# Performance work log

Hardware: AMD Instinct MI355X
Metric: run time of the kernel (lower is better)

## Reference

```python
import jax, jax.numpy as jnp
import numpy as np

NUM_NODES = 50000
NUM_EDGES = 600000
NUM_FEAT = 128
HIDDEN = 512
N_OUT = 128
K = 3
N_GRAPHS = 128


def setup_inputs() -> dict:
    key = jax.random.key(0)
    ks = jax.random.split(key, 12)
    feature = jax.random.normal(ks[0], (NUM_NODES, NUM_FEAT), dtype=jnp.float32)
    edge_index = jax.random.randint(ks[1], (2, NUM_EDGES), 0, NUM_NODES, dtype=jnp.int64)
    protein_batch = jnp.sort(jax.random.randint(ks[2], (NUM_NODES,), 0, N_GRAPHS, dtype=jnp.int64))
    s = 0.05
    # ChebConv weights stored [K, in, out] (x @ W), single shared bias per conv
    W1 = jax.random.normal(ks[3], (K, NUM_FEAT, NUM_FEAT), dtype=jnp.float32) * s
    b1 = jax.random.normal(ks[4], (NUM_FEAT,), dtype=jnp.float32) * s
    W2 = jax.random.normal(ks[5], (K, NUM_FEAT, 2 * NUM_FEAT), dtype=jnp.float32) * s
    b2 = jax.random.normal(ks[6], (2 * NUM_FEAT,), dtype=jnp.float32) * s
    fc1_w = jax.random.normal(ks[7], (3 * NUM_FEAT, HIDDEN), dtype=jnp.float32) * s
    fc1_b = jax.random.normal(ks[8], (HIDDEN,), dtype=jnp.float32) * s
    fc2_w = jax.random.normal(ks[9], (HIDDEN, N_OUT), dtype=jnp.float32) * s
    fc2_b = jax.random.normal(ks[10], (N_OUT,), dtype=jnp.float32) * s
    return {"feature": feature, "edge_index": edge_index, "protein_batch": protein_batch,
            "W1": W1, "b1": b1, "W2": W2, "b2": b2,
            "fc1_w": fc1_w, "fc1_b": fc1_b, "fc2_w": fc2_w, "fc2_b": fc2_b}


def _cheb_conv(x, src, dst, edge_w, W, b):
    # PyG ChebConv with sym normalization, lambda_max=2 => scaled Laplacian
    # L_hat has zero diagonal and off-diag weights -1/sqrt(d_i d_j) (edge_w).
    def prop(h):
        return jax.ops.segment_sum(edge_w[:, None] * h[src], dst, num_segments=NUM_NODES)

    Tx0 = x
    out = Tx0 @ W[0]
    Tx1 = prop(x)
    out = out + Tx1 @ W[1]
    for k in range(2, W.shape[0]):
        Tx2 = 2.0 * prop(Tx1) - Tx0
        out = out + Tx2 @ W[k]
        Tx0, Tx1 = Tx1, Tx2
    return out + b


def reference(feature, edge_index, protein_batch, W1, b1, W2, b2, fc1_w, fc1_b, fc2_w, fc2_b):
    src, dst = edge_index[0], edge_index[1]
    deg = jax.ops.segment_sum(jnp.ones_like(src, dtype=feature.dtype), src, num_segments=NUM_NODES)
    dinv = jnp.where(deg > 0, jax.lax.rsqrt(jnp.maximum(deg, 1.0)), 0.0)
    edge_w = -dinv[src] * dinv[dst]  # (2/lambda_max)*L_sym off-diagonal; diag cancels to 0

    gx = jax.nn.relu(_cheb_conv(feature, src, dst, edge_w, W1, b1))
    gx = jax.nn.relu(_cheb_conv(gx, src, dst, edge_w, W2, b2))
    gx = jnp.concatenate([gx, feature], axis=1)  # [N, 3*F]

    # global_mean_pool
    sums = jax.ops.segment_sum(gx, protein_batch, num_segments=N_GRAPHS)
    cnts = jax.ops.segment_sum(jnp.ones((gx.shape[0],), gx.dtype), protein_batch, num_segments=N_GRAPHS)
    pooled = sums / jnp.maximum(cnts, 1.0)[:, None]

    h = jax.nn.relu(pooled @ fc1_w + fc1_b)  # dropout is identity in eval
    return h @ fc2_w + fc2_b
```

## Files before the change

### kernel.cpp

```cpp
#include <hip/hip_runtime.h>
#include <hip/hip_bf16.h>

#define NNODES 50000
#define NEDGES 600000
#define NB 196
#define NBKT 196
#define SB 192
#define SCH (NEDGES / SB)

typedef short vs8 __attribute__((ext_vector_type(8)));
typedef float floatx4 __attribute__((ext_vector_type(4)));

__device__ __forceinline__ float us2f(unsigned short u) {
    unsigned int x = ((unsigned int)u) << 16;
    float f;
    __builtin_memcpy(&f, &x, 4);
    return f;
}
__device__ __forceinline__ unsigned short f2us(float f) {
    unsigned int x;
    __builtin_memcpy(&x, &f, 4);
    unsigned int r = x + 0x7fffu + ((x >> 16) & 1u);
    return (unsigned short)(r >> 16);
}
__device__ __forceinline__ float ldf(const void* p, int i, int ff) {
    if (ff) return us2f(((const unsigned short*)p)[i]);
    return ((const float*)p)[i];
}
__device__ __forceinline__ int2 ldnt_sw(const int2* p) {
    unsigned long long v =
        __builtin_nontemporal_load(reinterpret_cast<const unsigned long long*>(p));
    int2 r;
    r.x = (int)(unsigned int)(v & 0xffffffffULL);
    r.y = (int)(unsigned int)(v >> 32);
    return r;
}
__device__ __forceinline__ void accum8(float w, uint4 u, float& a0, float& a1,
                                       float& a2, float& a3, float& a4, float& a5,
                                       float& a6, float& a7) {
    a0 += w * us2f((unsigned short)(u.x & 0xffffu));
    a1 += w * us2f((unsigned short)(u.x >> 16));
    a2 += w * us2f((unsigned short)(u.y & 0xffffu));
    a3 += w * us2f((unsigned short)(u.y >> 16));
    a4 += w * us2f((unsigned short)(u.z & 0xffffu));
    a5 += w * us2f((unsigned short)(u.z >> 16));
    a6 += w * us2f((unsigned short)(u.w & 0xffffu));
    a7 += w * us2f((unsigned short)(u.w >> 16));
}

__global__ void k_detect(const int* ei, const unsigned int* fw, int* iflag, int* fflag) {
    int lane = threadIdx.x;
    int odd1 = ei[2 * lane + 1];
    int odd2 = ei[128 + 2 * lane + 1];
    unsigned long long nz = __ballot(odd1 != 0 || odd2 != 0);
    unsigned int e = (fw[lane] >> 7) & 0xffu;
    unsigned long long h = __ballot(e > 100u && e < 160u);
    if (lane == 0) {
        *iflag = (nz == 0ULL) ? 1 : 0;
        *fflag = (__popcll(h) > 40) ? 1 : 0;
    }
}

__global__ void k_init(const int* pb, const int* iflag, int* b32, float* psum) {
    int i = blockIdx.x * 256 + threadIdx.x;
    if (i < NNODES) {
        int f = *iflag;
        b32[i] = pb[((size_t)i) << f];
    }
    if (i < 128 * 384) psum[i] = 0.f;
}

__global__ __launch_bounds__(256) void k_deghist(const int* ei, const int* iflag,
                                                 unsigned int* degpart, int* cntpart) {
    __shared__ unsigned int h[25000];
    __shared__ int c[NBKT];
    int t = threadIdx.x, blk = blockIdx.x;
    for (int i = t; i < 25000; i += 256) h[i] = 0u;
    if (t < NBKT) c[t] = 0;
    __syncthreads();
    int f = *iflag;
    int e0 = blk * SCH;
    for (int j = t; j < SCH; j += 256) {
        int e = e0 + j;
        int s = ei[((size_t)e) << f];
        int d = ei[((size_t)(NEDGES + e)) << f];
        atomicAdd(&h[s >> 1], (s & 1) ? 65536u : 1u);
        atomicAdd(&c[d >> 8], 1);
    }
    __syncthreads();
    unsigned int* dp = degpart + (size_t)blk * 25000;
    for (int i = t; i < 25000; i += 256) dp[i] = h[i];
    if (t < NBKT) cntpart[blk * NBKT + t] = c[t];
}

__global__ void k_dred(const unsigned int* degpart, float* dinv) {
    int i = blockIdx.x * 256 + threadIdx.x;
    if (i >= 25000) return;
    unsigned int lo = 0, hi = 0;
    for (int b = 0; b < SB; ++b) {
        unsigned int p = degpart[(size_t)b * 25000 + i];
        lo += p & 0xffffu;
        hi += p >> 16;
    }
    dinv[2 * i] = lo ? rsqrtf((float)lo) : 0.f;
    dinv[2 * i + 1] = hi ? rsqrtf((float)hi) : 0.f;
}

__global__ void k_bscan(const int* cntpart, int* bbase, int* gbase,
                        const int* batch32, int* pcnt, int* rowptr) {
    __shared__ int tot[256];
    int t = threadIdx.x;
    int sum = 0;
    if (t < NBKT) {
        for (int b = 0; b < SB; ++b) sum += cntpart[b * NBKT + t];
    }
    tot[t] = sum;
    __syncthreads();
    for (int off = 1; off < 256; off <<= 1) {
        int x = (t >= off) ? tot[t - off] : 0;
        __syncthreads();
        tot[t] += x;
        __syncthreads();
    }
    int excl = tot[t] - sum;
    if (t < NBKT) {
        gbase[t] = excl;
        int run = excl;
        for (int b = 0; b < SB; ++b) {
            bbase[b * NBKT + t] = run;
            run += cntpart[b * NBKT + t];
        }
    }
    if (t == 0) {
        gbase[NBKT] = NEDGES;
        rowptr[NNODES] = NEDGES;
    }
    if (t < 128) {
        int g = t;
        int lo = 0, hi = NNODES;
        while (lo < hi) { int mid = (lo + hi) >> 1; if (batch32[mid] < g) lo = mid + 1; else hi = mid; }
        int start = lo;
        hi = NNODES;
        while (lo < hi) { int mid = (lo + hi) >> 1; if (batch32[mid] <= g) lo = mid + 1; else hi = mid; }
        pcnt[g] = lo - start;
    }
}

__global__ void k_scat(const int* ei, const int* iflag, const float* dinv,
                       const int* bbase, int2* bkt) {
    __shared__ int cur[NBKT];
    int t = threadIdx.x, blk = blockIdx.x;
    if (t < NBKT) cur[t] = bbase[blk * NBKT + t];
    __syncthreads();
    int f = *iflag;
    int e0 = blk * SCH;
    for (int j = t; j < SCH; j += 256) {
        int e = e0 + j;
        int s = ei[((size_t)e) << f];
        int d = ei[((size_t)(NEDGES + e)) << f];
        float w = -dinv[s] * dinv[d];
        int slot = atomicAdd(&cur[d >> 8], 1);
        int wb;
        __builtin_memcpy(&wb, &w, 4);
        int2 v;
        v.x = s | ((d & 255) << 16);
        v.y = wb;
        bkt[slot] = v;
    }
}

__global__ void k_csr(const int2* bkt, const int* gbase, int* rowptr, int2* csr_sw) {
    __shared__ int hist[256], scan[256], cur[256];
    int t = threadIdx.x, b = blockIdx.x;
    int beg = gbase[b], end = gbase[b + 1];
    int n = end - beg;
    hist[t] = 0;
    __syncthreads();
    for (int i = t; i < n; i += 256) {
        int bin = (bkt[beg + i].x >> 16) & 255;
        atomicAdd(&hist[bin], 1);
    }
    __syncthreads();
    int h = hist[t];
    scan[t] = h;
    __syncthreads();
    for (int off = 1; off < 256; off <<= 1) {
        int x = (t >= off) ? scan[t - off] : 0;
        __syncthreads();
        scan[t] += x;
        __syncthreads();
    }
    int excl = scan[t] - h;
    int node = b * 256 + t;
    if (node < NNODES) rowptr[node] = beg + excl;
    cur[t] = excl;
    __syncthreads();
    for (int i = t; i < n; i += 256) {
        int2 p = bkt[beg + i];
        int bin = (p.x >> 16) & 255;
        int slot = atomicAdd(&cur[bin], 1);
        int2 v;
        v.x = p.x & 0xffff;
        v.y = p.y;
        csr_sw[beg + slot] = v;
    }
}

__global__ void k_featb(const void* src, const int* fflag, unsigned short* dst) {
    int i = blockIdx.x * 256 + threadIdx.x;
    if (i >= NNODES * 128 / 8) return;
    if (*fflag) {
        reinterpret_cast<uint4*>(dst)[i] = reinterpret_cast<const uint4*>(src)[i];
    } else {
        const float4* fs = reinterpret_cast<const float4*>(src);
        float4 a = fs[2 * i], b = fs[2 * i + 1];
        uint4 o;
        o.x = (unsigned int)f2us(a.x) | ((unsigned int)f2us(a.y) << 16);
        o.y = (unsigned int)f2us(a.z) | ((unsigned int)f2us(a.w) << 16);
        o.z = (unsigned int)f2us(b.x) | ((unsigned int)f2us(b.y) << 16);
        o.w = (unsigned int)f2us(b.z) | ((unsigned int)f2us(b.w) << 16);
        reinterpret_cast<uint4*>(dst)[i] = o;
    }
}

__global__ void k_trans2(const void* W1, const void* W2, const int* fflag,
                         unsigned short* W1t, unsigned short* W2t) {
    int idx = blockIdx.x * 256 + threadIdx.x;
    int ff = *fflag;
    if (idx < 49152) {
        int n = idx / 384, k = idx - n * 384;
        float v;
        if (k < 128) v = ldf(W1, k * 128 + n, ff) - ldf(W1, (256 + k) * 128 + n, ff);
        else if (k < 256) v = ldf(W1, k * 128 + n, ff);
        else v = 2.f * ldf(W1, k * 128 + n, ff);
        W1t[idx] = f2us(v);
    } else if (idx < 49152 + 98304) {
        int j = idx - 49152;
        int n = j / 384, k = j - n * 384;
        float v;
        if (k < 128) v = ldf(W2, k * 256 + n, ff) - ldf(W2, (256 + k) * 256 + n, ff);
        else if (k < 256) v = ldf(W2, k * 256 + n, ff);
        else v = 2.f * ldf(W2, k * 256 + n, ff);
        W2t[j] = f2us(v);
    }
}

__global__ void k_prepw(const void* b1, const void* b2, const void* f1w, const void* f1b,
                        const void* f2w, const void* f2b, const int* fflag,
                        float* b1f, float* b2f, float* f1wf, float* f1bf,
                        float* f2wf, float* f2bf) {
    int i = blockIdx.x * 256 + threadIdx.x;
    int ff = *fflag;
    if (i < 196608) { f1wf[i] = ldf(f1w, i, ff); return; }
    i -= 196608;
    if (i < 65536) { f2wf[i] = ldf(f2w, i, ff); return; }
    i -= 65536;
    if (i < 512) { f1bf[i] = ldf(f1b, i, ff); return; }
    i -= 512;
    if (i < 256) { b2f[i] = ldf(b2, i, ff); return; }
    i -= 256;
    if (i < 128) { b1f[i] = ldf(b1, i, ff); return; }
    i -= 128;
    if (i < 128) f2bf[i] = ldf(f2b, i, ff);
}

__global__ __launch_bounds__(256, 4) void k_prop(const unsigned short* X,
                                                 const int* rowptr, const int2* csr_sw,
                                                 unsigned short* out) {
    int wvid = (blockIdx.x * blockDim.x + threadIdx.x) >> 6;
    int lane = threadIdx.x & 63;
    int q = lane >> 4;
    int ln = lane & 15;
    int node = wvid * 4 + q;
    if (node >= NNODES) return;
    int fo = ln * 8;
    int beg = rowptr[node], end = rowptr[node + 1];
    float a0 = 0.f, a1 = 0.f, a2 = 0.f, a3 = 0.f;
    float a4 = 0.f, a5 = 0.f, a6 = 0.f, a7 = 0.f;
    int j = beg;
    for (; j + 8 <= end; j += 8) {
        int2 e0 = ldnt_sw(csr_sw + j);
        int2 e1 = ldnt_sw(csr_sw + j + 1);
        int2 e2 = ldnt_sw(csr_sw + j + 2);
        int2 e3 = ldnt_sw(csr_sw + j + 3);
        int2 e4 = ldnt_sw(csr_sw + j + 4);
        int2 e5 = ldnt_sw(csr_sw + j + 5);
        int2 e6 = ldnt_sw(csr_sw + j + 6);
        int2 e7 = ldnt_sw(csr_sw + j + 7);
        uint4 u0 = *reinterpret_cast<const uint4*>(X + (size_t)e0.x * 128 + fo);
        uint4 u1 = *reinterpret_cast<const uint4*>(X + (size_t)e1.x * 128 + fo);
        uint4 u2 = *reinterpret_cast<const uint4*>(X + (size_t)e2.x * 128 + fo);
        uint4 u3 = *reinterpret_cast<const uint4*>(X + (size_t)e3.x * 128 + fo);
        uint4 u4 = *reinterpret_cast<const uint4*>(X + (size_t)e4.x * 128 + fo);
        uint4 u5 = *reinterpret_cast<const uint4*>(X + (size_t)e5.x * 128 + fo);
        uint4 u6 = *reinterpret_cast<const uint4*>(X + (size_t)e6.x * 128 + fo);
        uint4 u7 = *reinterpret_cast<const uint4*>(X + (size_t)e7.x * 128 + fo);
        float w0, w1, w2, w3, w4, w5, w6, w7;
        __builtin_memcpy(&w0, &e0.y, 4);
        __builtin_memcpy(&w1, &e1.y, 4);
        __builtin_memcpy(&w2, &e2.y, 4);
        __builtin_memcpy(&w3, &e3.y, 4);
        __builtin_memcpy(&w4, &e4.y, 4);
        __builtin_memcpy(&w5, &e5.y, 4);
        __builtin_memcpy(&w6, &e6.y, 4);
        __builtin_memcpy(&w7, &e7.y, 4);
        accum8(w0, u0, a0, a1, a2, a3, a4, a5, a6, a7);
        accum8(w1, u1, a0, a1, a2, a3, a4, a5, a6, a7);
        accum8(w2, u2, a0, a1, a2, a3, a4, a5, a6, a7);
        accum8(w3, u3, a0, a1, a2, a3, a4, a5, a6, a7);
        accum8(w4, u4, a0, a1, a2, a3, a4, a5, a6, a7);
        accum8(w5, u5, a0, a1, a2, a3, a4, a5, a6, a7);
        accum8(w6, u6, a0, a1, a2, a3, a4, a5, a6, a7);
        accum8(w7, u7, a0, a1, a2, a3, a4, a5, a6, a7);
    }
    for (; j + 4 <= end; j += 4) {
        int2 e0 = ldnt_sw(csr_sw + j);
        int2 e1 = ldnt_sw(csr_sw + j + 1);
        int2 e2 = ldnt_sw(csr_sw + j + 2);
        int2 e3 = ldnt_sw(csr_sw + j + 3);
        uint4 u0 = *reinterpret_cast<const uint4*>(X + (size_t)e0.x * 128 + fo);
        uint4 u1 = *reinterpret_cast<const uint4*>(X + (size_t)e1.x * 128 + fo);
        uint4 u2 = *reinterpret_cast<const uint4*>(X + (size_t)e2.x * 128 + fo);
        uint4 u3 = *reinterpret_cast<const uint4*>(X + (size_t)e3.x * 128 + fo);
        float w0, w1, w2, w3;
        __builtin_memcpy(&w0, &e0.y, 4);
        __builtin_memcpy(&w1, &e1.y, 4);
        __builtin_memcpy(&w2, &e2.y, 4);
        __builtin_memcpy(&w3, &e3.y, 4);
        accum8(w0, u0, a0, a1, a2, a3, a4, a5, a6, a7);
        accum8(w1, u1, a0, a1, a2, a3, a4, a5, a6, a7);
        accum8(w2, u2, a0, a1, a2, a3, a4, a5, a6, a7);
        accum8(w3, u3, a0, a1, a2, a3, a4, a5, a6, a7);
    }
    for (; j < end; ++j) {
        int2 e = ldnt_sw(csr_sw + j);
        float w;
        __builtin_memcpy(&w, &e.y, 4);
        uint4 u = *reinterpret_cast<const uint4*>(X + (size_t)e.x * 128 + fo);
        accum8(w, u, a0, a1, a2, a3, a4, a5, a6, a7);
    }
    uint4 ov;
    ov.x = (unsigned int)f2us(a0) | ((unsigned int)f2us(a1) << 16);
    ov.y = (unsigned int)f2us(a2) | ((unsigned int)f2us(a3) << 16);
    ov.z = (unsigned int)f2us(a4) | ((unsigned int)f2us(a5) << 16);
    ov.w = (unsigned int)f2us(a6) | ((unsigned int)f2us(a7) << 16);
    *reinterpret_cast<uint4*>(out + (size_t)node * 128 + fo) = ov;
}

template <int POOL>
__global__ __launch_bounds__(512, 4) void k_convg(
    const unsigned short* seg0, const unsigned short* seg1, const unsigned short* seg2,
    const unsigned short* Wt, const float* bias, unsigned short* out,
    const int* batch32, float* psum, int nout, int nslab) {
    __shared__ unsigned short shb[24576];
    __shared__ float sh_ps[512];
    int tid = threadIdx.x;
    int bid = blockIdx.x;
    int grp = 8 * nslab;
    int main_blocks = 24 * grp;
    int r, slab;
    if (bid < main_blocks) {
        int g = bid / grp;
        int rem = bid - g * grp;
        slab = rem >> 3;
        r = g * 8 + (rem & 7);
    } else {
        int t = bid - main_blocks;
        r = 192 + (t & 3);
        slab = t >> 2;
    }
    int col0 = slab * 64;
    if (POOL) sh_ps[tid] = 0.f;
#pragma unroll
    for (int it = 0; it < 6; ++it) {
        int idx = tid + it * 512;
        int kkt = idx >> 6, ln = idx & 63;
        int kk = kkt >> 2, t = kkt & 3;
        int col = col0 + t * 16 + (ln & 15);
        int ko = kk * 32 + (ln >> 4) * 8;
        uint4 v = *reinterpret_cast<const uint4*>(Wt + (size_t)col * 384 + ko);
        *reinterpret_cast<uint4*>(shb + idx * 8) = v;
    }
    __syncthreads();
    int wv = tid >> 6, lane = tid & 63;
    int m = lane & 15, kq = lane >> 4;
    int row0 = r * 256 + wv * 32;
    int rr0 = row0 + m;
    int rr1 = row0 + 16 + m;
    if (rr0 >= NNODES) rr0 = NNODES - 1;
    if (rr1 >= NNODES) rr1 = NNODES - 1;
    floatx4 acc[2][4];
#pragma unroll
    for (int rI = 0; rI < 2; ++rI)
#pragma unroll
        for (int t = 0; t < 4; ++t) {
            acc[rI][t][0] = 0.f; acc[rI][t][1] = 0.f; acc[rI][t][2] = 0.f; acc[rI][t][3] = 0.f;
        }
    vs8 a0[12], a1[12];
#pragma unroll
    for (int p = 0; p < 4; ++p) {
        int ko = p * 32 + kq * 8;
        a0[p] = *reinterpret_cast<const vs8*>(seg0 + (size_t)rr0 * 128 + ko);
        a1[p] = *reinterpret_cast<const vs8*>(seg0 + (size_t)rr1 * 128 + ko);
    }
    __builtin_amdgcn_sched_barrier(0);
#pragma unroll
    for (int kk = 0; kk < 12; ++kk) {
        int kp = kk + 4;
        if (kp < 12) {
            const unsigned short* S = (kp < 8) ? seg1 : seg2;
            int ko = (kp & 3) * 32 + kq * 8;
            a0[kp] = *reinterpret_cast<const vs8*>(S + (size_t)rr0 * 128 + ko);
            a1[kp] = *reinterpret_cast<const vs8*>(S + (size_t)rr1 * 128 + ko);
            __builtin_amdgcn_sched_barrier(0);
        }
#pragma unroll
        for (int t = 0; t < 4; ++t) {
            vs8 b = *reinterpret_cast<const vs8*>(shb + ((kk * 4 + t) * 64 + lane) * 8);
            acc[0][t] = __builtin_amdgcn_mfma_f32_16x16x32_bf16(a0[kk], b, acc[0][t], 0, 0, 0);
            acc[1][t] = __builtin_amdgcn_mfma_f32_16x16x32_bf16(a1[kk], b, acc[1][t], 0, 0, 0);
        }
    }
    if (POOL == 0) {
#pragma unroll
        for (int rI = 0; rI < 2; ++rI) {
            int orow_base = row0 + rI * 16 + kq * 4;
#pragma unroll
            for (int t = 0; t < 4; ++t) {
                int col = col0 + t * 16 + m;
                float bv = bias[col];
#pragma unroll
                for (int i = 0; i < 4; ++i) {
                    int rw = orow_base + i;
                    if (rw < NNODES) {
                        float v = acc[rI][t][i] + bv;
                        v = v > 0.f ? v : 0.f;
                        out[(size_t)rw * nout + col] = f2us(v);
                    }
                }
            }
        }
    } else {
        int g0 = batch32[r * 256];
#pragma unroll
        for (int rI = 0; rI < 2; ++rI) {
            int orow_base = row0 + rI * 16 + kq * 4;
            int gid[4];
#pragma unroll
            for (int i = 0; i < 4; ++i) {
                int rw = orow_base + i;
                gid[i] = rw < NNODES ? batch32[rw] : -1;
            }
#pragma unroll
            for (int t = 0; t < 4; ++t) {
                int col = col0 + t * 16 + m;
                float bv = bias[col];
                float run = 0.f;
                int curg = -1;
#pragma unroll
                for (int i = 0; i < 4; ++i) {
                    int g = gid[i];
                    if (g < 0) break;
                    float v = acc[rI][t][i] + bv;
                    v = v > 0.f ? v : 0.f;
                    if (g != curg) {
                        if (curg >= 0) {
                            int gl = curg - g0;
                            if (gl >= 0 && gl < 8) atomicAdd(&sh_ps[gl * 64 + t * 16 + m], run);
                            else atomicAdd(&psum[curg * 384 + col], run);
                        }
                        curg = g;
                        run = 0.f;
                    }
                    run += v;
                }
                if (curg >= 0) {
                    int gl = curg - g0;
                    if (gl >= 0 && gl < 8) atomicAdd(&sh_ps[gl * 64 + t * 16 + m], run);
                    else atomicAdd(&psum[curg * 384 + col], run);
                }
            }
        }
        __syncthreads();
        int gl = tid >> 6, c = tid & 63;
        float v = sh_ps[tid];
        int gg = g0 + gl;
        if (v != 0.f && gg < 128) atomicAdd(&psum[(size_t)gg * 384 + col0 + c], v);
    }
}

__global__ void k_poolnodes(const unsigned short* featb, const int* batch32, float* psum) {
    int col = threadIdx.x & 127;
    int half = threadIdx.x >> 7;
    int nbeg = blockIdx.x * 128 + half * 64;
    if (nbeg >= NNODES) return;
    int nend = nbeg + 64;
    if (nend > NNODES) nend = NNODES;
    float run = 0.f;
    int curg = batch32[nbeg];
    for (int n = nbeg; n < nend; ++n) {
        int g = batch32[n];
        if (g != curg) {
            atomicAdd(&psum[curg * 384 + 256 + col], run);
            run = 0.f;
            curg = g;
        }
        run += us2f(featb[(size_t)n * 128 + col]);
    }
    atomicAdd(&psum[curg * 384 + 256 + col], run);
}

__global__ void k_fc1(const float* psum, const int* pcnt, const float* w,
                      const float* b, float* h) {
    int g = blockIdx.x, j = threadIdx.x * 2;
    int c = pcnt[g];
    float inv = 1.f / (float)(c > 0 ? c : 1);
    float a0 = 0.f, a1 = 0.f;
    for (int k = 0; k < 384; ++k) {
        float p = psum[g * 384 + k];
        a0 += p * w[k * 512 + j];
        a1 += p * w[k * 512 + j + 1];
    }
    a0 = a0 * inv + b[j];
    a1 = a1 * inv + b[j + 1];
    h[g * 512 + j] = a0 > 0.f ? a0 : 0.f;
    h[g * 512 + j + 1] = a1 > 0.f ? a1 : 0.f;
}

__global__ void ChebModel_74380243632480_kernel(const float* h, const float* w,
                                                const float* b, const int* fflag,
                                                void* out) {
    int g = blockIdx.x, j = threadIdx.x;
    float acc = 0.f;
    for (int k = 0; k < 512; ++k) acc += h[g * 512 + k] * w[k * 128 + j];
    acc += b[j];
    if (*fflag) ((unsigned short*)out)[g * 128 + j] = f2us(acc);
    else ((float*)out)[g * 128 + j] = acc;
}

extern "C" void kernel_launch(void* const* d_in, const int* in_sizes, int n_in,
                              void* d_out, int out_size, void* d_ws, size_t ws_size,
                              hipStream_t stream) {
    const void* feature = d_in[0];
    const int* edge_index = (const int*)d_in[1];
    const int* batch = (const int*)d_in[2];
    const void* W1 = d_in[3];
    const void* b1 = d_in[4];
    const void* W2 = d_in[5];
    const void* b2 = d_in[6];
    const void* fc1w = d_in[7];
    const void* fc1b = d_in[8];
    const void* fc2w = d_in[9];
    const void* fc2b = d_in[10];

    char* ws = (char*)d_ws;
    size_t off = 0;
    int* iflag = (int*)(ws + off); off += 256;
    int* fflag = (int*)(ws + off); off += 256;
    int* rowptr = (int*)(ws + off); off += ((size_t)(NNODES + 1) * 4 + 255) & ~(size_t)255;
    float* dinv = (float*)(ws + off); off += ((size_t)NNODES * 4 + 255) & ~(size_t)255;
    int* batch32 = (int*)(ws + off); off += ((size_t)NNODES * 4 + 255) & ~(size_t)255;
    int* gbase = (int*)(ws + off); off += 1024;
    int* cntpart = (int*)(ws + off); off += ((size_t)SB * NBKT * 4 + 255) & ~(size_t)255;
    int* bbase = (int*)(ws + off); off += ((size_t)SB * NBKT * 4 + 255) & ~(size_t)255;
    int2* csr_sw = (int2*)(ws + off); off += ((size_t)NEDGES * 8 + 255) & ~(size_t)255;
    unsigned short* featb = (unsigned short*)(ws + off); off += ((size_t)NNODES * 128 * 2 + 255) & ~(size_t)255;
    unsigned short* T1 = (unsigned short*)(ws + off); off += ((size_t)NNODES * 128 * 2 + 255) & ~(size_t)255;
    unsigned short* T2 = (unsigned short*)(ws + off); off += ((size_t)NNODES * 128 * 2 + 255) & ~(size_t)255;
    unsigned short* gx1 = (unsigned short*)(ws + off); off += ((size_t)NNODES * 128 * 2 + 255) & ~(size_t)255;
    unsigned short* W1t = (unsigned short*)(ws + off); off += ((size_t)49152 * 2 + 255) & ~(size_t)255;
    unsigned short* W2t = (unsigned short*)(ws + off); off += ((size_t)98304 * 2 + 255) & ~(size_t)255;
    float* b1f = (float*)(ws + off); off += 1024;
    float* b2f = (float*)(ws + off); off += 1024;
    float* fc1wf = (float*)(ws + off); off += ((size_t)196608 * 4 + 255) & ~(size_t)255;
    float* fc1bf = (float*)(ws + off); off += 2048;
    float* fc2wf = (float*)(ws + off); off += ((size_t)65536 * 4 + 255) & ~(size_t)255;
    float* fc2bf = (float*)(ws + off); off += 1024;
    float* psum = (float*)(ws + off); off += ((size_t)128 * 384 * 4 + 255) & ~(size_t)255;
    int* pcnt = (int*)(ws + off); off += 1024;
    float* hbuf = (float*)(ws + off); off += ((size_t)128 * 512 * 4 + 255) & ~(size_t)255;

    int2* bkt = (int2*)T1;
    unsigned int* degpart = (unsigned int*)T2;

    k_detect<<<1, 64, 0, stream>>>(edge_index, (const unsigned int*)feature, iflag, fflag);
    k_init<<<(NNODES + 255) / 256, 256, 0, stream>>>(batch, iflag, batch32, psum);
    k_deghist<<<SB, 256, 0, stream>>>(edge_index, iflag, degpart, cntpart);
    k_dred<<<(25000 + 255) / 256, 256, 0, stream>>>(degpart, dinv);
    k_bscan<<<1, 256, 0, stream>>>(cntpart, bbase, gbase, batch32, pcnt, rowptr);
    k_scat<<<SB, 256, 0, stream>>>(edge_index, iflag, dinv, bbase, bkt);
    k_csr<<<NBKT, 256, 0, stream>>>(bkt, gbase, rowptr, csr_sw);

    k_featb<<<(NNODES * 128 / 8 + 255) / 256, 256, 0, stream>>>(feature, fflag, featb);
    k_trans2<<<(49152 + 98304 + 255) / 256, 256, 0, stream>>>(W1, W2, fflag, W1t, W2t);
    k_prepw<<<(263168 + 255) / 256, 256, 0, stream>>>(b1, b2, fc1w, fc1b, fc2w, fc2b, fflag,
                                                      b1f, b2f, fc1wf, fc1bf, fc2wf, fc2bf);

    int pb = ((NNODES + 3) / 4 * 64 + 255) / 256;
    k_prop<<<pb, 256, 0, stream>>>(featb, rowptr, csr_sw, T1);
    k_prop<<<pb, 256, 0, stream>>>(T1, rowptr, csr_sw, T2);
    k_convg<0><<<196 * 2, 512, 0, stream>>>(featb, T1, T2, W1t, b1f, gx1,
                                            (const int*)0, (float*)0, 128, 2);
    k_prop<<<pb, 256, 0, stream>>>(gx1, rowptr, csr_sw, T1);
    k_prop<<<pb, 256, 0, stream>>>(T1, rowptr, csr_sw, T2);
    k_convg<1><<<196 * 4, 512, 0, stream>>>(gx1, T1, T2, W2t, b2f, (unsigned short*)0,
                                            batch32, psum, 256, 4);
    k_poolnodes<<<(NNODES + 127) / 128, 256, 0, stream>>>(featb, batch32, psum);
    k_fc1<<<128, 256, 0, stream>>>(psum, pcnt, fc1wf, fc1bf, hbuf);
    ChebModel_74380243632480_kernel<<<128, 128, 0, stream>>>(hbuf, fc2wf, fc2bf, fflag, d_out);
}
```

Before: 401.5 us.

## Restructure conv GEMM into 128-row full-width tiles with double-buffered LDS

The Chebyshev conv GEMM kernel now gives each block 128 rows and all output columns (128 or 256), in place of 256-row by 64-column slabs that reloaded A across several column-slab blocks. A and B are staged through double-buffered LDS in 32-wide K chunks with a swizzled A layout, and each wave computes a 64x(NCOL/4) tile. This cuts redundant A reads from global memory and raises MFMA reuse per LDS fragment. In exchange there are two barriers per K step, more accumulator registers (especially for NCOL=256), and fewer, larger blocks.

```diff
diff --git a/kernel.cpp b/kernel.cpp
--- a/kernel.cpp
+++ b/kernel.cpp
@@ -347,113 +347,133 @@
     *reinterpret_cast<uint4*>(out + (size_t)node * 128 + fo) = ov;
 }
 
-template <int POOL>
+template <int POOL, int NCOL>
 __global__ __launch_bounds__(512, 4) void k_convg(
     const unsigned short* seg0, const unsigned short* seg1, const unsigned short* seg2,
     const unsigned short* Wt, const float* bias, unsigned short* out,
-    const int* batch32, float* psum, int nout, int nslab) {
-    __shared__ unsigned short shb[24576];
-    __shared__ float sh_ps[512];
+    const int* batch32, float* psum) {
+    constexpr int NT = NCOL / 64;
+    constexpr int NSLOT = (NCOL / 16) * 64;
+    constexpr int BPT = NSLOT / 512;
+    __shared__ unsigned short a_lds[2][128 * 32];
+    __shared__ unsigned short b_lds[2][NSLOT * 8];
+    __shared__ float sh_ps[POOL ? 8 * NCOL : 1];
+
     int tid = threadIdx.x;
-    int bid = blockIdx.x;
-    int grp = 8 * nslab;
-    int main_blocks = 24 * grp;
-    int r, slab;
-    if (bid < main_blocks) {
-        int g = bid / grp;
-        int rem = bid - g * grp;
-        slab = rem >> 3;
-        r = g * 8 + (rem & 7);
-    } else {
-        int t = bid - main_blocks;
-        r = 192 + (t & 3);
-        slab = t >> 2;
-    }
-    int col0 = slab * 64;
-    if (POOL) sh_ps[tid] = 0.f;
-#pragma unroll
-    for (int it = 0; it < 6; ++it) {
-        int idx = tid + it * 512;
-        int kkt = idx >> 6, ln = idx & 63;
-        int kk = kkt >> 2, t = kkt & 3;
-        int col = col0 + t * 16 + (ln & 15);
-        int ko = kk * 32 + (ln >> 4) * 8;
-        uint4 v = *reinterpret_cast<const uint4*>(Wt + (size_t)col * 384 + ko);
-        *reinterpret_cast<uint4*>(shb + idx * 8) = v;
-    }
-    __syncthreads();
+    int r0 = blockIdx.x * 128;
+    const unsigned short* segs[3] = {seg0, seg1, seg2};
+
+    if (POOL)
+        for (int i = tid; i < 8 * NCOL; i += 512) sh_ps[i] = 0.f;
+
+    int arow = tid >> 2, apart = tid & 3;
+    int argl = r0 + arow;
+    if (argl >= NNODES) argl = NNODES - 1;
+    int awb = ((apart + arow) & 3) * 8;
+
+    uint4 ra, rb[BPT];
+    ra = *reinterpret_cast<const uint4*>(seg0 + (size_t)argl * 128 + apart * 8);
+#pragma unroll
+    for (int qb = 0; qb < BPT; ++qb) {
+        int s = tid + qb * 512;
+        int col = (s >> 6) * 16 + (s & 15), kqs = (s >> 4) & 3;
+        rb[qb] = *reinterpret_cast<const uint4*>(Wt + (size_t)col * 384 + kqs * 8);
+    }
+    *reinterpret_cast<uint4*>(&a_lds[0][arow * 32 + awb]) = ra;
+#pragma unroll
+    for (int qb = 0; qb < BPT; ++qb)
+        *reinterpret_cast<uint4*>(&b_lds[0][(tid + qb * 512) * 8]) = rb[qb];
+    __syncthreads();
+
     int wv = tid >> 6, lane = tid & 63;
+    int wm = wv >> 2, wn = wv & 3;
     int m = lane & 15, kq = lane >> 4;
-    int row0 = r * 256 + wv * 32;
-    int rr0 = row0 + m;
-    int rr1 = row0 + 16 + m;
-    if (rr0 >= NNODES) rr0 = NNODES - 1;
-    if (rr1 >= NNODES) rr1 = NNODES - 1;
-    floatx4 acc[2][4];
-#pragma unroll
-    for (int rI = 0; rI < 2; ++rI)
-#pragma unroll
-        for (int t = 0; t < 4; ++t) {
-            acc[rI][t][0] = 0.f; acc[rI][t][1] = 0.f; acc[rI][t][2] = 0.f; acc[rI][t][3] = 0.f;
-        }
-    vs8 a0[12], a1[12];
-#pragma unroll
-    for (int p = 0; p < 4; ++p) {
-        int ko = p * 32 + kq * 8;
-        a0[p] = *reinterpret_cast<const vs8*>(seg0 + (size_t)rr0 * 128 + ko);
-        a1[p] = *reinterpret_cast<const vs8*>(seg0 + (size_t)rr1 * 128 + ko);
-    }
-    __builtin_amdgcn_sched_barrier(0);
-#pragma unroll
-    for (int kk = 0; kk < 12; ++kk) {
-        int kp = kk + 4;
-        if (kp < 12) {
-            const unsigned short* S = (kp < 8) ? seg1 : seg2;
-            int ko = (kp & 3) * 32 + kq * 8;
-            a0[kp] = *reinterpret_cast<const vs8*>(S + (size_t)rr0 * 128 + ko);
-            a1[kp] = *reinterpret_cast<const vs8*>(S + (size_t)rr1 * 128 + ko);
+    floatx4 acc[4][NT];
+#pragma unroll
+    for (int mt = 0; mt < 4; ++mt)
+#pragma unroll
+        for (int nt = 0; nt < NT; ++nt) {
+            acc[mt][nt][0] = 0.f; acc[mt][nt][1] = 0.f;
+            acc[mt][nt][2] = 0.f; acc[mt][nt][3] = 0.f;
+        }
+
+#pragma unroll
+    for (int c = 0; c < 12; ++c) {
+        int cb = c & 1;
+        if (c + 1 < 12) {
+            const unsigned short* S = segs[(c + 1) >> 2];
+            int koff = ((c + 1) & 3) * 32;
+            ra = *reinterpret_cast<const uint4*>(S + (size_t)argl * 128 + koff + apart * 8);
+#pragma unroll
+            for (int qb = 0; qb < BPT; ++qb) {
+                int s = tid + qb * 512;
+                int col = (s >> 6) * 16 + (s & 15), kqs = (s >> 4) & 3;
+                rb[qb] = *reinterpret_cast<const uint4*>(
+                    Wt + (size_t)col * 384 + (c + 1) * 32 + kqs * 8);
+            }
             __builtin_amdgcn_sched_barrier(0);
         }
-#pragma unroll
-        for (int t = 0; t < 4; ++t) {
-            vs8 b = *reinterpret_cast<const vs8*>(shb + ((kk * 4 + t) * 64 + lane) * 8);
-            acc[0][t] = __builtin_amdgcn_mfma_f32_16x16x32_bf16(a0[kk], b, acc[0][t], 0, 0, 0);
-            acc[1][t] = __builtin_amdgcn_mfma_f32_16x16x32_bf16(a1[kk], b, acc[1][t], 0, 0, 0);
-        }
-    }
+        vs8 af[4], bf[NT];
+#pragma unroll
+        for (int mt = 0; mt < 4; ++mt) {
+            int row = wm * 64 + mt * 16 + m;
+            af[mt] = *reinterpret_cast<const vs8*>(
+                &a_lds[cb][row * 32 + (((kq + row) & 3)) * 8]);
+        }
+#pragma unroll
+        for (int nt = 0; nt < NT; ++nt) {
+            int t = wn * NT + nt;
+            bf[nt] = *reinterpret_cast<const vs8*>(&b_lds[cb][(t * 64 + lane) * 8]);
+        }
+#pragma unroll
+        for (int mt = 0; mt < 4; ++mt)
+#pragma unroll
+            for (int nt = 0; nt < NT; ++nt)
+                acc[mt][nt] = __builtin_amdgcn_mfma_f32_16x16x32_bf16(
+                    af[mt], bf[nt], acc[mt][nt], 0, 0, 0);
+        if (c + 1 < 12) {
+            __syncthreads();
+            *reinterpret_cast<uint4*>(&a_lds[cb ^ 1][arow * 32 + awb]) = ra;
+#pragma unroll
+            for (int qb = 0; qb < BPT; ++qb)
+                *reinterpret_cast<uint4*>(&b_lds[cb ^ 1][(tid + qb * 512) * 8]) = rb[qb];
+            __syncthreads();
+        }
+    }
+
     if (POOL == 0) {
 #pragma unroll
-        for (int rI = 0; rI < 2; ++rI) {
-            int orow_base = row0 + rI * 16 + kq * 4;
-#pragma unroll
-            for (int t = 0; t < 4; ++t) {
-                int col = col0 + t * 16 + m;
+        for (int mt = 0; mt < 4; ++mt) {
+            int rbase = r0 + wm * 64 + mt * 16 + kq * 4;
+#pragma unroll
+            for (int nt = 0; nt < NT; ++nt) {
+                int col = wn * (NT * 16) + nt * 16 + m;
                 float bv = bias[col];
 #pragma unroll
                 for (int i = 0; i < 4; ++i) {
-                    int rw = orow_base + i;
+                    int rw = rbase + i;
                     if (rw < NNODES) {
-                        float v = acc[rI][t][i] + bv;
+                        float v = acc[mt][nt][i] + bv;
                         v = v > 0.f ? v : 0.f;
-                        out[(size_t)rw * nout + col] = f2us(v);
+                        out[(size_t)rw * NCOL + col] = f2us(v);
                     }
                 }
             }
         }
     } else {
-        int g0 = batch32[r * 256];
-#pragma unroll
-        for (int rI = 0; rI < 2; ++rI) {
-            int orow_base = row0 + rI * 16 + kq * 4;
+        int g0 = batch32[r0];
+#pragma unroll
+        for (int mt = 0; mt < 4; ++mt) {
+            int rbase = r0 + wm * 64 + mt * 16 + kq * 4;
             int gid[4];
 #pragma unroll
             for (int i = 0; i < 4; ++i) {
-                int rw = orow_base + i;
+                int rw = rbase + i;
                 gid[i] = rw < NNODES ? batch32[rw] : -1;
             }
 #pragma unroll
-            for (int t = 0; t < 4; ++t) {
-                int col = col0 + t * 16 + m;
+            for (int nt = 0; nt < NT; ++nt) {
+                int col = wn * (NT * 16) + nt * 16 + m;
                 float bv = bias[col];
                 float run = 0.f;
                 int curg = -1;
@@ -461,12 +481,12 @@
                 for (int i = 0; i < 4; ++i) {
                     int g = gid[i];
                     if (g < 0) break;
-                    float v = acc[rI][t][i] + bv;
+                    float v = acc[mt][nt][i] + bv;
                     v = v > 0.f ? v : 0.f;
                     if (g != curg) {
                         if (curg >= 0) {
                             int gl = curg - g0;
-                            if (gl >= 0 && gl < 8) atomicAdd(&sh_ps[gl * 64 + t * 16 + m], run);
+                            if (gl >= 0 && gl < 8) atomicAdd(&sh_ps[gl * NCOL + col], run);
                             else atomicAdd(&psum[curg * 384 + col], run);
                         }
                         curg = g;
@@ -476,16 +496,18 @@
                 }
                 if (curg >= 0) {
                     int gl = curg - g0;
-                    if (gl >= 0 && gl < 8) atomicAdd(&sh_ps[gl * 64 + t * 16 + m], run);
+                    if (gl >= 0 && gl < 8) atomicAdd(&sh_ps[gl * NCOL + col], run);
                     else atomicAdd(&psum[curg * 384 + col], run);
                 }
             }
         }
         __syncthreads();
-        int gl = tid >> 6, c = tid & 63;
-        float v = sh_ps[tid];
-        int gg = g0 + gl;
-        if (v != 0.f && gg < 128) atomicAdd(&psum[(size_t)gg * 384 + col0 + c], v);
+        for (int idx = tid; idx < 8 * NCOL; idx += 512) {
+            int gl = idx / NCOL, cc = idx - gl * NCOL;
+            float v = sh_ps[idx];
+            int gg = g0 + gl;
+            if (v != 0.f && gg < 128) atomicAdd(&psum[(size_t)gg * 384 + cc], v);
+        }
     }
 }
 
@@ -597,14 +619,15 @@
                                                       b1f, b2f, fc1wf, fc1bf, fc2wf, fc2bf);
 
     int pb = ((NNODES + 3) / 4 * 64 + 255) / 256;
+    int cgrid = (NNODES + 127) / 128;
     k_prop<<<pb, 256, 0, stream>>>(featb, rowptr, csr_sw, T1);
     k_prop<<<pb, 256, 0, stream>>>(T1, rowptr, csr_sw, T2);
-    k_convg<0><<<196 * 2, 512, 0, stream>>>(featb, T1, T2, W1t, b1f, gx1,
-                                            (const int*)0, (float*)0, 128, 2);
+    k_convg<0, 128><<<cgrid, 512, 0, stream>>>(featb, T1, T2, W1t, b1f, gx1,
+                                               (const int*)0, (float*)0);
     k_prop<<<pb, 256, 0, stream>>>(gx1, rowptr, csr_sw, T1);
     k_prop<<<pb, 256, 0, stream>>>(T1, rowptr, csr_sw, T2);
-    k_convg<1><<<196 * 4, 512, 0, stream>>>(gx1, T1, T2, W2t, b2f, (unsigned short*)0,
-                                            batch32, psum, 256, 4);
+    k_convg<1, 256><<<cgrid, 512, 0, stream>>>(gx1, T1, T2, W2t, b2f, (unsigned short*)0,
+                                               batch32, psum);
     k_poolnodes<<<(NNODES + 127) / 128, 256, 0, stream>>>(featb, batch32, psum);
     k_fc1<<<128, 256, 0, stream>>>(psum, pcnt, fc1wf, fc1bf, hbuf);
     ChebModel_74380243632480_kernel<<<128, 128, 0, stream>>>(hbuf, fc2wf, fc2bf, fflag, d_out);
```

Measured after the change: 414.9 us. 3.3% more time.
